# Optimization experiments

Hardware: AMD Instinct MI355X
Metric: run time of the kernel (lower is better)

## Reference

```python
import jax, jax.numpy as jnp
import numpy as np

B, T, DM = 4, 2048, 1024
H, DK, DV = 16, 64, 64


def setup_inputs() -> dict:
    key = jax.random.key(0)
    k1, k2, k3, k4 = jax.random.split(key, 4)
    x = jax.random.normal(k1, (B, T, DM), dtype=jnp.float32)
    scale = 0.02
    Wq = jax.random.normal(k2, (H, DM, DK), dtype=jnp.float32) * scale
    Wk = jax.random.normal(k3, (H, DM, DK), dtype=jnp.float32) * scale
    Wv = jax.random.normal(k4, (H, DM, DV), dtype=jnp.float32) * scale
    return {"x": x, "Wq": Wq, "Wk": Wk, "Wv": Wv}


def reference(x, Wq, Wk, Wv):
    # Per-head projections, vectorized over heads: [B,H,T,dk]
    q = jnp.einsum('btd,hdk->bhtk', x, Wq)
    k = jnp.einsum('btd,hdk->bhtk', x, Wk)
    v = jnp.einsum('btd,hdv->bhtv', x, Wv)
    scale = DK ** -0.5  # k.shape[-1] ** -0.5 in original
    wei = jnp.einsum('bhtk,bhsk->bhts', q, k) * scale  # [B,H,T,T]
    causal = jnp.tril(jnp.ones((T, T), dtype=bool))
    wei = jnp.where(causal, wei, -jnp.inf)
    wei = jax.nn.softmax(wei, axis=-1)
    # dropout p=0.0 -> identity (eval-mode equivalent)
    out = jnp.einsum('bhts,bhsv->bhtv', wei, v)  # [B,H,T,dv]
    # concat heads along last dim: [B,T,H*dv]
    return out.transpose(0, 2, 1, 3).reshape(B, T, H * DV)
```

## Files before the change

kernel.cpp:

```cpp
#include <hip/hip_runtime.h>


#define B_  4
#define T_  2048
#define DM_ 1024
#define H_  16
#define D_  64
#define DMO 1024

typedef unsigned short u16;
typedef unsigned int   u32;
typedef u16   u16x8  __attribute__((ext_vector_type(8)));
typedef short s16x8  __attribute__((ext_vector_type(8)));
typedef float f32x4  __attribute__((ext_vector_type(4)));
typedef float f32x16 __attribute__((ext_vector_type(16)));
typedef u32   u32x2  __attribute__((ext_vector_type(2)));
typedef u32   u32x4  __attribute__((ext_vector_type(4)));

#if __has_builtin(__builtin_amdgcn_exp2f)
#define EXP2(x) __builtin_amdgcn_exp2f(x)
#else
#define EXP2(x) __expf((x) * 0.69314718f)
#endif

__device__ __forceinline__ u16 f2bf_hu(float f) {
    u32 u = __builtin_bit_cast(u32, f) + 0x8000u;
    return (u16)(u >> 16);
}
__device__ __forceinline__ u32 pk2(float lo, float hi) {
    u32 ul = __builtin_bit_cast(u32, lo) + 0x8000u;
    u32 uh = __builtin_bit_cast(u32, hi) + 0x8000u;
    return __builtin_amdgcn_perm(uh, ul, 0x07060302);
}
__device__ __forceinline__ u16x8 cvt8(const float* s) {
    f32x4 a = *(const f32x4*)s;
    f32x4 b = *(const f32x4*)(s + 4);
    u32x4 r { pk2(a[0], a[1]), pk2(a[2], a[3]), pk2(b[0], b[1]), pk2(b[2], b[3]) };
    return __builtin_bit_cast(u16x8, r);
}
__device__ __forceinline__ f32x4 mfma16(u16x8 a, u16x8 b, f32x4 c) {
    return __builtin_amdgcn_mfma_f32_16x16x32_bf16(
        __builtin_bit_cast(s16x8, a), __builtin_bit_cast(s16x8, b), c, 0, 0, 0);
}
__device__ __forceinline__ f32x16 mfma32(u16x8 a, u16x8 b, f32x16 c) {
    return __builtin_amdgcn_mfma_f32_32x32x16_bf16(
        __builtin_bit_cast(s16x8, a), __builtin_bit_cast(s16x8, b), c, 0, 0, 0);
}
__device__ __forceinline__ void gld_lds16(const u16* g, u16* l) {
    __builtin_amdgcn_global_load_lds(
        (const __attribute__((address_space(1))) u32*)g,
        (__attribute__((address_space(3))) u32*)l, 16, 0, 0);
}

__global__ __launch_bounds__(256) void cvt_all(
    const float* __restrict__ x,  const float* __restrict__ Wq,
    const float* __restrict__ Wk, const float* __restrict__ Wv,
    u16* __restrict__ xb, u16* __restrict__ Wt)
{
    __shared__ u16 L[64][74];
    const int bx = blockIdx.x;
    if (bx < 1024) {
        size_t i0 = ((size_t)bx * 256 + threadIdx.x) * 32;
        #pragma unroll
        for (int c = 0; c < 4; c++)
            *(u16x8*)(xb + i0 + c * 8) = cvt8(x + i0 + c * 8);
        return;
    }
    const int wb = bx - 1024;
    const int dblk = wb & 15, h = (wb >> 4) & 15, mat = wb >> 8;
    const float* W = (mat == 0) ? Wq : (mat == 1) ? Wk : Wv;
    const int tid = threadIdx.x;
    {
        const int dl = tid >> 2, c = (tid & 3) * 16;
        const float* src = W + ((size_t)h * DM_ + dblk * 64 + dl) * D_ + c;
        #pragma unroll
        for (int g = 0; g < 2; g++)
            *(u16x8*)&L[dl][c + g * 8] = cvt8(src + g * 8);
    }
    __syncthreads();
    {
        const int dkr = tid >> 2, g = tid & 3;
        u16 tmp[16];
        #pragma unroll
        for (int j = 0; j < 16; j++) tmp[j] = L[g * 16 + j][dkr];
        u16* dst = Wt + ((size_t)(mat * 16 + h) * 64 + dkr) * DM_ + dblk * 64 + g * 16;
        *(u16x8*)dst = *(u16x8*)tmp;
        *(u16x8*)(dst + 8) = *(u16x8*)(tmp + 8);
    }
}

template<int SWAP>
__device__ __forceinline__ void pcompute(const char* Asb, const char* Bsb,
                                         int wm, int wn, int quad, int l16,
                                         int ax, f32x4 (&acc)[4][4]) {
    #pragma unroll
    for (int ks = 0; ks < 2; ks++) {
        u16x8 af[4], bf[4];
        #pragma unroll
        for (int i = 0; i < 4; i++)
            af[i] = *(const u16x8*)(Asb +
                ((((wm * 64 + i * 16 + l16) * 64 + ks * 32 + quad * 8) * 2) ^ ax));
        #pragma unroll
        for (int j = 0; j < 4; j++)
            bf[j] = *(const u16x8*)(Bsb +
                ((((wn * 64 + j * 16 + l16) * 64 + ks * 32 + quad * 8) * 2) ^ ax));
        #pragma unroll
        for (int i = 0; i < 4; i++)
            #pragma unroll
            for (int j = 0; j < 4; j++)
                acc[i][j] = SWAP ? mfma16(bf[j], af[i], acc[i][j])
                                 : mfma16(af[i], bf[j], acc[i][j]);
    }
}

__global__ __launch_bounds__(256) void proj_kernel(
    const u16* __restrict__ xb, const u16* __restrict__ Wt,
    u16* __restrict__ Qc, u16* __restrict__ Kc, u16* __restrict__ Vtc)
{
    __shared__ __attribute__((aligned(16))) u16 As0[128][64];
    __shared__ __attribute__((aligned(16))) u16 Bs0[128][64];
    __shared__ __attribute__((aligned(16))) u16 As1[128][64];
    __shared__ __attribute__((aligned(16))) u16 Bs1[128][64];

    const int pb = blockIdx.x;
    const int wg = (pb & 7) * 192 + (pb >> 3);
    const int m0 = (wg & 63) * 128;
    const int n0 = (wg >> 6) * 128;
    const int mat = n0 >> 10;
    const int tid  = threadIdx.x;
    const int wave = tid >> 6, lane = tid & 63;
    const int quad = lane >> 4, l16 = lane & 15;
    const int wm   = wave >> 1, wn = wave & 1;

    const int r8 = lane >> 3, g8 = lane & 7;
    const int gs = (g8 ^ r8) * 8;
    const int ax = (l16 & 7) << 4;

    f32x4 acc[4][4];
    #pragma unroll
    for (int i = 0; i < 4; i++)
        #pragma unroll
        for (int j = 0; j < 4; j++) acc[i][j] = f32x4{0.f, 0.f, 0.f, 0.f};

    auto STAGE = [&](u16* Ad, u16* Bd, int kb) {
        const int kbase = kb * 64;
        #pragma unroll
        for (int it = 0; it < 4; it++) {
            const int row = it * 32 + wave * 8 + r8;
            const int ldo = (it * 4 + wave) * 512 + lane * 8;
            gld_lds16(xb + (size_t)(m0 + row) * DM_ + kbase + gs, Ad + ldo);
            gld_lds16(Wt + (size_t)(n0 + row) * DM_ + kbase + gs, Bd + ldo);
        }
    };

    STAGE(&As0[0][0], &Bs0[0][0], 0);
    __syncthreads();

    #define PLOOP(SW)                                                        \
        for (int kb = 0; kb < 16; kb += 2) {                                 \
            STAGE(&As1[0][0], &Bs1[0][0], kb + 1);                           \
            pcompute<SW>((const char*)As0, (const char*)Bs0,                 \
                         wm, wn, quad, l16, ax, acc);                        \
            __syncthreads();                                                 \
            if (kb + 2 < 16) STAGE(&As0[0][0], &Bs0[0][0], kb + 2);          \
            pcompute<SW>((const char*)As1, (const char*)Bs1,                 \
                         wm, wn, quad, l16, ax, acc);                        \
            __syncthreads();                                                 \
        }
    if (mat != 2) { PLOOP(1) } else { PLOOP(0) }
    #undef PLOOP

    const int h_base = (n0 & 1023) >> 6;
    if (mat != 2) {
        u16* Cm = (mat == 0) ? Qc : Kc;
        const float sc = (mat == 0) ? 0.18033688f : 1.0f;
        #pragma unroll
        for (int i = 0; i < 4; i++) {
            const int m  = m0 + wm * 64 + i * 16 + l16;
            const int bb = m >> 11, t = m & (T_ - 1);
            u16* rowp = Cm + ((size_t)(bb * H_ + h_base + wn) * T_ + t) * D_;
            #pragma unroll
            for (int j = 0; j < 4; j++) {
                const int dk0 = j * 16 + quad * 4;
                u32x2 d { pk2(acc[i][j][0] * sc, acc[i][j][1] * sc),
                          pk2(acc[i][j][2] * sc, acc[i][j][3] * sc) };
                *(u32x2*)(rowp + dk0) = d;
            }
        }
    } else {
        #pragma unroll
        for (int i = 0; i < 4; i++) {
            const int m  = m0 + wm * 64 + i * 16 + quad * 4;
            const int bb = m >> 11, t = m & (T_ - 1);
            #pragma unroll
            for (int j = 0; j < 4; j++) {
                const int dk = j * 16 + l16;
                u32x2 d { pk2(acc[i][j][0], acc[i][j][1]),
                          pk2(acc[i][j][2], acc[i][j][3]) };
                *(u32x2*)(Vtc + ((size_t)(bb * H_ + h_base + wn) * D_ + dk) * T_ + t) = d;
            }
        }
    }
}

__global__ __launch_bounds__(128, 2) void attn_kernel(
    const u16* __restrict__ Qc, const u16* __restrict__ Kc,
    const u16* __restrict__ Vtc, float* __restrict__ out)
{
    __shared__ __attribute__((aligned(16))) u16 Ks[2][64][64];
    __shared__ __attribute__((aligned(16))) u16 Vs[2][64][64];

    const int pb = blockIdx.x;
    const int lb = (pb & 7) * 128 + (pb >> 3);
    const int pr = lb & 15;
    const int bh = lb >> 4;
    const int h  = bh & 15, b = bh >> 4;
    const int qa = pr, qb = 31 - pr;

    const int tid = threadIdx.x, w = tid >> 6, lane = tid & 63;
    const int l31 = lane & 31, hi = lane >> 5;
    const int r8 = lane >> 3, g8 = lane & 7;
    const int gs = (g8 ^ r8) * 8;
    const int ax = (l31 & 7) << 4;
    const int qloc = w * 32 + l31;

    const u16* Qbh = Qc + (size_t)(b * H_ + h) * T_ * D_;
    const u16* Kbh = Kc + (size_t)(b * H_ + h) * T_ * D_;
    const u16* Vbh = Vtc + (size_t)(b * H_ + h) * D_ * T_;

    auto STAGE = [&](int buf, int t) {
        const int sbase = t * 64;
        u16* Kd = &Ks[buf][0][0];
        u16* Vd = &Vs[buf][0][0];
        #pragma unroll
        for (int i2 = 0; i2 < 4; i2++) {
            const int seg = i2 * 2 + w;
            const int row = seg * 8 + r8;
            const int ldo = seg * 512 + lane * 8;
            gld_lds16(Kbh + (size_t)(sbase + row) * D_ + gs, Kd + ldo);
            gld_lds16(Vbh + (size_t)row * T_ + sbase + gs,  Vd + ldo);
        }
    };

    int qrow = qa * 64 + qloc;
    u16x8 qf[4];
    #pragma unroll
    for (int ks = 0; ks < 4; ks++)
        qf[ks] = *(const u16x8*)(Qbh + (size_t)qrow * D_ + ks * 16 + hi * 8);

    f32x16 ot0, ot1;
    #pragma unroll
    for (int r = 0; r < 16; r++) { ot0[r] = 0.f; ot1[r] = 0.f; }
    float mi = -1e30f, li = 0.f;

    auto EPI = [&]() {
        const float inv = 1.0f / li;
        float* orow = out + (size_t)(b * T_ + qrow) * DMO + h * D_;
        #pragma unroll
        for (int c = 0; c < 2; c++)
            #pragma unroll
            for (int hf = 0; hf < 2; hf++) {
                f32x4 v0, v1;
                #pragma unroll
                for (int j = 0; j < 4; j++) {
                    v0[j] = ot0[c * 8 + hf * 4 + j] * inv;
                    v1[j] = ot1[c * 8 + hf * 4 + j] * inv;
                }
                *(f32x4*)(orow + c * 16 + hf * 8 + hi * 4)      = v0;
                *(f32x4*)(orow + 32 + c * 16 + hf * 8 + hi * 4) = v1;
            }
    };

    STAGE(0, 0);
    __syncthreads();
    int cur = 0;

    for (int i = 0; i <= 32; i++) {
        if (i < 32) {
            const int nx = i + 1;
            const int tn = (nx <= qa) ? nx : nx - qa - 1;
            STAGE(cur ^ 1, tn);
        }
        const char* Ksb = (const char*)&Ks[cur][0][0];
        const char* Vsb = (const char*)&Vs[cur][0][0];

        f32x16 st0, st1;
        #pragma unroll
        for (int r = 0; r < 16; r++) { st0[r] = 0.f; st1[r] = 0.f; }
        __builtin_amdgcn_s_setprio(1);
        #pragma unroll
        for (int ks = 0; ks < 4; ks++) {
            const int co = (ks * 16 + hi * 8) * 2;
            u16x8 k0 = *(const u16x8*)(Ksb + ((l31 * 128 + co) ^ ax));
            u16x8 k1 = *(const u16x8*)(Ksb + (((32 + l31) * 128 + co) ^ ax));
            st0 = mfma32(k0, qf[ks], st0);
            st1 = mfma32(k1, qf[ks], st1);
        }
        __builtin_amdgcn_s_setprio(0);

        if (i == qa || i == 32) {
            #pragma unroll
            for (int r = 0; r < 16; r++) {
                const int sl = (r & 3) + 8 * (r >> 2) + 4 * hi;
                if (sl > qloc)      st0[r] = -1e30f;
                if (sl + 32 > qloc) st1[r] = -1e30f;
            }
        }

        float mx = -1e30f;
        #pragma unroll
        for (int r = 0; r < 16; r++) mx = fmaxf(mx, fmaxf(st0[r], st1[r]));
        mx = fmaxf(mx, __shfl_xor(mx, 32));
        if (!__all(mx - mi <= 8.f)) {
            const float mn = fmaxf(mi, mx);
            const float al = EXP2(mi - mn);
            li *= al;
            #pragma unroll
            for (int r = 0; r < 16; r++) { ot0[r] *= al; ot1[r] *= al; }
            mi = mn;
        }
        float sum = 0.f;
        #pragma unroll
        for (int r = 0; r < 16; r++) {
            const float p0 = EXP2(st0[r] - mi);
            const float p1 = EXP2(st1[r] - mi);
            st0[r] = p0; st1[r] = p1;
            sum += p0 + p1;
        }
        sum += __shfl_xor(sum, 32);
        li += sum;

        u16x8 pb4[4];
        #define PACK(SRC, C, OUT) {                                           \
            u32 d0 = pk2(SRC[8*(C)+0], SRC[8*(C)+1]);                         \
            u32 d1 = pk2(SRC[8*(C)+2], SRC[8*(C)+3]);                         \
            u32 d2 = pk2(SRC[8*(C)+4], SRC[8*(C)+5]);                         \
            u32 d3 = pk2(SRC[8*(C)+6], SRC[8*(C)+7]);                         \
            u32 e0 = __shfl_xor(hi ? d0 : d2, 32);                            \
            u32 e1 = __shfl_xor(hi ? d1 : d3, 32);                            \
            u32x4 wds{ hi ? e0 : d0, hi ? e1 : d1,                            \
                       hi ? d2 : e0, hi ? d3 : e1 };                          \
            OUT = __builtin_bit_cast(u16x8, wds); }
        PACK(st0, 0, pb4[0]); PACK(st0, 1, pb4[1]);
        PACK(st1, 0, pb4[2]); PACK(st1, 1, pb4[3]);
        #undef PACK

        __builtin_amdgcn_s_setprio(1);
        #pragma unroll
        for (int kc = 0; kc < 4; kc++) {
            const int co = (kc * 16 + hi * 8) * 2;
            u16x8 v0 = *(const u16x8*)(Vsb + ((l31 * 128 + co) ^ ax));
            u16x8 v1 = *(const u16x8*)(Vsb + (((32 + l31) * 128 + co) ^ ax));
            ot0 = mfma32(v0, pb4[kc], ot0);
            ot1 = mfma32(v1, pb4[kc], ot1);
        }
        __builtin_amdgcn_s_setprio(0);

        if (i == qa) {
            EPI();
            qrow = qb * 64 + qloc;
            #pragma unroll
            for (int ks = 0; ks < 4; ks++)
                qf[ks] = *(const u16x8*)(Qbh + (size_t)qrow * D_ + ks * 16 + hi * 8);
            #pragma unroll
            for (int r = 0; r < 16; r++) { ot0[r] = 0.f; ot1[r] = 0.f; }
            mi = -1e30f; li = 0.f;
        }
        __syncthreads();
        cur ^= 1;
    }
    EPI();
}

extern "C" void kernel_launch(void* const* d_in, const int* in_sizes, int n_in,
                              void* d_out, int out_size, void* d_ws, size_t ws_size,
                              hipStream_t stream) {
    int xi = 0, wi[3] = {1, 2, 3};
    {
        int k = 0, found = 0;
        for (int i = 0; i < n_in && i < 8; i++) {
            if (in_sizes[i] == B_ * T_ * DM_) { xi = i; found = 1; }
            else if (in_sizes[i] == H_ * DM_ * D_ && k < 3) wi[k++] = i;
        }
        if (!found || k != 3) { xi = 0; wi[0] = 1; wi[1] = 2; wi[2] = 3; }
    }
    const float* x  = (const float*)d_in[xi];
    const float* Wq = (const float*)d_in[wi[0]];
    const float* Wk = (const float*)d_in[wi[1]];
    const float* Wv = (const float*)d_in[wi[2]];
    float* out = (float*)d_out;

    u16* xb = (u16*)d_out;
    u16* Wt = xb + (size_t)B_ * T_ * DM_;
    const size_t per = (size_t)B_ * H_ * T_ * D_;
    u16* Qc  = (u16*)d_ws;
    u16* Kc  = Qc + per;
    u16* Vtc = Kc + per;

    cvt_all<<<1792, 256, 0, stream>>>(x, Wq, Wk, Wv, xb, Wt);
    proj_kernel<<<1536, 256, 0, stream>>>(xb, Wt, Qc, Kc, Vtc);
    attn_kernel<<<1024, 128, 0, stream>>>(Qc, Kc, Vtc, out);
}
```

Baseline: 240.2 us.

## Deepen load pipeline with vmcnt-counted waits in projection and attention kernels

Both kernels now issue the next two shared-memory tile loads up front. Each step waits with `s_waitcnt vmcnt(8)` plus a raw barrier instead of `__syncthreads`, which drained every outstanding global load. The loop is unrolled by two over fixed buffers, so one stage of loads stays in flight while the other buffer is being computed. The projection kernel also raises wave priority around its MFMA block. The vmcnt counting relies on exact per-stage load counts, and other outstanding memory ops (the Q reloads and output stores) make the waits more conservative.

After: 233.0 us. 1.03x faster.

```diff
diff --git a/kernel.cpp b/kernel.cpp
--- a/kernel.cpp
+++ b/kernel.cpp
@@ -22,6 +22,14 @@
 #else
 #define EXP2(x) __expf((x) * 0.69314718f)
 #endif
+
+#define WAIT_BAR(N) do {                                                      \
+    asm volatile("s_waitcnt vmcnt(" #N ")" ::: "memory");                     \
+    __builtin_amdgcn_s_barrier();                                             \
+    __builtin_amdgcn_sched_barrier(0); } while (0)
+#define BAR_ONLY() do {                                                       \
+    __builtin_amdgcn_s_barrier();                                             \
+    __builtin_amdgcn_sched_barrier(0); } while (0)
 
 __device__ __forceinline__ u16 f2bf_hu(float f) {
     u32 u = __builtin_bit_cast(u32, f) + 0x8000u;
@@ -104,12 +112,14 @@
         for (int j = 0; j < 4; j++)
             bf[j] = *(const u16x8*)(Bsb +
                 ((((wn * 64 + j * 16 + l16) * 64 + ks * 32 + quad * 8) * 2) ^ ax));
+        __builtin_amdgcn_s_setprio(1);
         #pragma unroll
         for (int i = 0; i < 4; i++)
             #pragma unroll
             for (int j = 0; j < 4; j++)
                 acc[i][j] = SWAP ? mfma16(bf[j], af[i], acc[i][j])
                                  : mfma16(af[i], bf[j], acc[i][j]);
+        __builtin_amdgcn_s_setprio(0);
     }
 }
 
@@ -154,18 +164,20 @@
     };
 
     STAGE(&As0[0][0], &Bs0[0][0], 0);
-    __syncthreads();
+    STAGE(&As1[0][0], &Bs1[0][0], 1);
 
     #define PLOOP(SW)                                                        \
-        for (int kb = 0; kb < 16; kb += 2) {                                 \
-            STAGE(&As1[0][0], &Bs1[0][0], kb + 1);                           \
+        for (int j = 0; j < 8; j++) {                                        \
+            WAIT_BAR(8);                                                     \
             pcompute<SW>((const char*)As0, (const char*)Bs0,                 \
                          wm, wn, quad, l16, ax, acc);                        \
-            __syncthreads();                                                 \
-            if (kb + 2 < 16) STAGE(&As0[0][0], &Bs0[0][0], kb + 2);          \
+            BAR_ONLY();                                                      \
+            if (2 * j + 2 < 16) STAGE(&As0[0][0], &Bs0[0][0], 2 * j + 2);    \
+            if (j < 7) { WAIT_BAR(8); } else { WAIT_BAR(0); }                \
             pcompute<SW>((const char*)As1, (const char*)Bs1,                 \
                          wm, wn, quad, l16, ax, acc);                        \
-            __syncthreads();                                                 \
+            BAR_ONLY();                                                      \
+            if (2 * j + 3 < 16) STAGE(&As1[0][0], &Bs1[0][0], 2 * j + 3);    \
         }
     if (mat != 2) { PLOOP(1) } else { PLOOP(0) }
     #undef PLOOP
@@ -207,8 +219,10 @@
     const u16* __restrict__ Qc, const u16* __restrict__ Kc,
     const u16* __restrict__ Vtc, float* __restrict__ out)
 {
-    __shared__ __attribute__((aligned(16))) u16 Ks[2][64][64];
-    __shared__ __attribute__((aligned(16))) u16 Vs[2][64][64];
+    __shared__ __attribute__((aligned(16))) u16 Ks0[64][64];
+    __shared__ __attribute__((aligned(16))) u16 Vs0[64][64];
+    __shared__ __attribute__((aligned(16))) u16 Ks1[64][64];
+    __shared__ __attribute__((aligned(16))) u16 Vs1[64][64];
 
     const int pb = blockIdx.x;
     const int lb = (pb & 7) * 128 + (pb >> 3);
@@ -228,10 +242,10 @@
     const u16* Kbh = Kc + (size_t)(b * H_ + h) * T_ * D_;
     const u16* Vbh = Vtc + (size_t)(b * H_ + h) * D_ * T_;
 
-    auto STAGE = [&](int buf, int t) {
+    auto TS = [&](int i) { return (i <= qa) ? i : i - qa - 1; };
+
+    auto STAGE = [&](u16* Kd, u16* Vd, int t) {
         const int sbase = t * 64;
-        u16* Kd = &Ks[buf][0][0];
-        u16* Vd = &Vs[buf][0][0];
         #pragma unroll
         for (int i2 = 0; i2 < 4; i2++) {
             const int seg = i2 * 2 + w;
@@ -271,19 +285,7 @@
             }
     };
 
-    STAGE(0, 0);
-    __syncthreads();
-    int cur = 0;
-
-    for (int i = 0; i <= 32; i++) {
-        if (i < 32) {
-            const int nx = i + 1;
-            const int tn = (nx <= qa) ? nx : nx - qa - 1;
-            STAGE(cur ^ 1, tn);
-        }
-        const char* Ksb = (const char*)&Ks[cur][0][0];
-        const char* Vsb = (const char*)&Vs[cur][0][0];
-
+    auto COMPUTE = [&](const char* Ksb, const char* Vsb, int i) {
         f32x16 st0, st1;
         #pragma unroll
         for (int r = 0; r < 16; r++) { st0[r] = 0.f; st1[r] = 0.f; }
@@ -366,9 +368,24 @@
             for (int r = 0; r < 16; r++) { ot0[r] = 0.f; ot1[r] = 0.f; }
             mi = -1e30f; li = 0.f;
         }
-        __syncthreads();
-        cur ^= 1;
-    }
+    };
+
+    STAGE(&Ks0[0][0], &Vs0[0][0], 0);
+    STAGE(&Ks1[0][0], &Vs1[0][0], TS(1));
+
+    for (int j = 0; j < 16; j++) {
+        const int i0 = 2 * j, i1 = 2 * j + 1;
+        WAIT_BAR(8);
+        COMPUTE((const char*)Ks0, (const char*)Vs0, i0);
+        BAR_ONLY();
+        if (i0 + 2 <= 32) STAGE(&Ks0[0][0], &Vs0[0][0], TS(i0 + 2));
+        WAIT_BAR(8);
+        COMPUTE((const char*)Ks1, (const char*)Vs1, i1);
+        BAR_ONLY();
+        if (i1 + 2 <= 32) STAGE(&Ks1[0][0], &Vs1[0][0], TS(i1 + 2));
+    }
+    WAIT_BAR(0);
+    COMPUTE((const char*)Ks0, (const char*)Vs0, 32);
     EPI();
 }
 
```
